# Kernel tuning notes

Measured on AMD Instinct MI355X. Metric: run time of the kernel, lower is better.

The kernel has to match this reference:

```python
import jax, jax.numpy as jnp
import numpy as np

ALPHA = 0.2   # LeakyReLU negative slope
NEG = -9e15   # mask fill value from the torch code


def _conv1d(x, w, b):
    # x: (N, C_in, L), w: (C_out, C_in, 5), padding=2 -> same length
    y = jax.lax.conv_general_dilated(x, w, window_strides=(1,), padding=[(2, 2)],
                                     dimension_numbers=('NCH', 'OIH', 'NCH'))
    return y + b[None, :, None]


def _gat(h, mask, W, a):
    # Faithful to a_input @ a: e_ij = leakyrelu(Wh_i . a[:H] + Wh_j . a[H:])
    Wh = jnp.einsum('bnf,fo->bno', h, W)          # (B,N,H)
    H = W.shape[1]
    f1 = Wh @ a[:H]                               # (B,N,1)
    f2 = Wh @ a[H:]                               # (B,N,1)
    e = f1 + jnp.swapaxes(f2, 1, 2)               # (B,N,N)
    e = jnp.where(e > 0, e, ALPHA * e)            # LeakyReLU
    e = jnp.where(mask, e, NEG)
    att = jax.nn.softmax(e, axis=-1)              # dropout skipped (eval mode)
    return jnp.einsum('bij,bjo->bio', att, Wh)


def setup_inputs() -> dict:
    key = jax.random.key(0)
    ks = jax.random.split(key, 14)
    B, S, N, H, E = 8, 200, 512, 64, 2048
    sc = 0.1
    return {
        'x': jax.random.normal(ks[0], (B, S, N * 2), dtype=jnp.float32),
        'adj': jax.random.randint(ks[1], (N, N), 0, 2, dtype=jnp.int32),
        'edge_index': jax.random.randint(ks[2], (E, 2), 0, N, dtype=jnp.int32),
        'conv1_w': jax.random.normal(ks[3], (H // 2, 2, 5), dtype=jnp.float32) * sc,
        'conv1_b': jnp.zeros((H // 2,), dtype=jnp.float32),
        'conv2_w': jax.random.normal(ks[4], (H, H // 2, 5), dtype=jnp.float32) * sc,
        'conv2_b': jnp.zeros((H,), dtype=jnp.float32),
        'W1': jax.random.normal(ks[5], (H, H), dtype=jnp.float32) * sc,
        'a1': jax.random.normal(ks[6], (2 * H, 1), dtype=jnp.float32) * sc,
        'W2': jax.random.normal(ks[7], (H, H), dtype=jnp.float32) * sc,
        'a2': jax.random.normal(ks[8], (2 * H, 1), dtype=jnp.float32) * sc,
        'fc1_w': jax.random.normal(ks[9], (2 * H, H), dtype=jnp.float32) * sc,
        'fc1_b': jnp.zeros((H,), dtype=jnp.float32),
        'fc2_w': jax.random.normal(ks[10], (H, 1), dtype=jnp.float32) * sc,
        'fc2_b': jnp.zeros((1,), dtype=jnp.float32),
    }


def reference(x, adj, edge_index, conv1_w, conv1_b, conv2_w, conv2_b,
              W1, a1, W2, a2, fc1_w, fc1_b, fc2_w, fc2_b):
    B = x.shape[0]
    N = adj.shape[0]
    # (B,S,2N) -> (B,N,S,2) -> (B*N,2,S)
    xn = x.reshape(B, -1, N, 2).transpose(0, 2, 1, 3)
    xf = xn.reshape(B * N, -1, 2).transpose(0, 2, 1)
    h = jax.nn.relu(_conv1d(xf, conv1_w, conv1_b))
    h = jax.nn.relu(_conv1d(h, conv2_w, conv2_b))
    h = h.mean(axis=-1)                 # AdaptiveAvgPool1d(1) + squeeze
    h = h.reshape(B, N, -1)             # (B,N,H)
    mask = (adj > 0)[None]              # (1,N,N) broadcasts over batch
    h = jax.nn.relu(_gat(h, mask, W1, a1))
    h = _gat(h, mask, W2, a2)
    h1 = h[:, edge_index[:, 0]]         # (B,E,H)
    h2 = h[:, edge_index[:, 1]]
    he = jnp.concatenate([h1, h2], axis=-1)  # (B,E,2H)
    z = jax.nn.relu(he @ fc1_w + fc1_b)
    return jax.nn.sigmoid(z @ fc2_w + fc2_b).squeeze(-1)  # (B,E)
```

## Files before the change

### kernel.cpp

```cpp
#include <hip/hip_runtime.h>

typedef unsigned short u16;
typedef __attribute__((ext_vector_type(8))) short short8;
typedef __attribute__((ext_vector_type(4))) float float4v;

#define BATCH 8
#define SLEN  200
#define NNODE 512
#define C1    32
#define C2    64
#define NEDGE 2048
#define NEGV  -9000000000000000.0f

#define H1S 40
#define H1R 212

__device__ __forceinline__ u16 f2bf(float f) {
    unsigned int x = __float_as_uint(f);
    unsigned int lsb = (x >> 16) & 1u;
    x += 0x7fffu + lsb;
    return (u16)(x >> 16);
}

__global__ __launch_bounds__(256) void conv_fused_kernel(
    const float* __restrict__ x,
    const float* __restrict__ w1,
    const float* __restrict__ b1,
    const float* __restrict__ w2,
    const float* __restrict__ b2,
    float* __restrict__ hmean)
{
    __shared__ float xs[2][SLEN + 4];
    __shared__ __align__(16) u16 h1p[H1R * H1S];

    const int t    = threadIdx.x;
    const int blk  = blockIdx.x;
    const int b    = blk >> 9;
    const int n    = blk & 511;
    const int lane = t & 63;
    const int wv   = t >> 6;
    const int ml   = lane & 15;
    const int q    = lane >> 4;

    short8 bfrag[5];
    {
        const float* wp = w2 + (size_t)(wv * 16 + ml) * 160 + (q * 8) * 5;
        #pragma unroll
        for (int kk = 0; kk < 5; ++kk) {
            #pragma unroll
            for (int j = 0; j < 8; ++j)
                bfrag[kk][j] = (short)f2bf(wp[j * 5 + kk]);
        }
    }
    const float bias2 = b2[wv * 16 + ml];

    if (t < SLEN) {
        const float* xp = x + ((size_t)(b * SLEN + t)) * (NNODE * 2) + n * 2;
        xs[0][2 + t] = xp[0];
        xs[1][2 + t] = xp[1];
    } else if (t < SLEN + 8) {
        int c = (t - SLEN) & 1;
        int p = (t - SLEN) >> 1;
        int pos = (p < 2) ? p : (SLEN + p);
        xs[c][pos] = 0.f;
    }
    {
        unsigned int* hz = (unsigned int*)h1p;
        if (t < 40)       hz[t] = 0u;
        else if (t < 240) hz[202 * (H1S / 2) + (t - 40)] = 0u;
    }
    __syncthreads();

    {
        const int p  = t >> 4;
        const int sg = t & 15;
        float wA[10], wB[10];
        #pragma unroll
        for (int j = 0; j < 10; ++j) {
            wA[j] = w1[(2 * p) * 10 + j];
            wB[j] = w1[(2 * p + 1) * 10 + j];
        }
        const float bA = b1[2 * p], bB = b1[2 * p + 1];
        for (int i = 0; i < 13; ++i) {
            const int s = sg + 16 * i;
            if (s < SLEN) {
                float a0 = bA, a1 = bB;
                #pragma unroll
                for (int k = 0; k < 5; ++k) {
                    const float x0 = xs[0][s + k], x1 = xs[1][s + k];
                    a0 += wA[k] * x0 + wA[5 + k] * x1;
                    a1 += wB[k] * x0 + wB[5 + k] * x1;
                }
                a0 = fmaxf(a0, 0.f);
                a1 = fmaxf(a1, 0.f);
                unsigned int pack = (unsigned int)f2bf(a0) | ((unsigned int)f2bf(a1) << 16);
                *(unsigned int*)&h1p[(2 + s) * H1S + 2 * p] = pack;
            }
        }
    }
    __syncthreads();

    float total = 0.f;
    for (int mt = 0; mt < 13; ++mt) {
        const int m0 = mt * 16;
        float4v acc = {0.f, 0.f, 0.f, 0.f};
        #pragma unroll
        for (int kk = 0; kk < 5; ++kk) {
            const short8 a = *(const short8*)&h1p[(m0 + ml + kk) * H1S + q * 8];
            acc = __builtin_amdgcn_mfma_f32_16x16x32_bf16(a, bfrag[kk], acc, 0, 0, 0);
        }
        #pragma unroll
        for (int r = 0; r < 4; ++r) {
            const int m = m0 + q * 4 + r;
            if (m < SLEN) total += fmaxf(acc[r] + bias2, 0.f);
        }
    }
    total += __shfl_xor(total, 16, 64);
    total += __shfl_xor(total, 32, 64);
    if (lane < 16)
        hmean[(size_t)blk * 64 + wv * 16 + lane] = total * (1.0f / 200.0f);
}

__global__ __launch_bounds__(256) void gat_wh_kernel(
    const float* __restrict__ h,
    const float* __restrict__ W,
    const float* __restrict__ a,
    u16* __restrict__ Wh_bt,
    float* __restrict__ f1,
    float* __restrict__ f2)
{
    __shared__ __align__(16) u16 hA[64 * 72];
    __shared__ __align__(16) u16 Wt[64 * 72];
    __shared__ __align__(16) u16 whT[64 * 72];
    __shared__ float as[128];

    const int t    = threadIdx.x;
    const int blk  = blockIdx.x;
    const int b    = blk >> 3;
    const int j0   = (blk & 7) * 64;
    const int lane = t & 63, wv = t >> 6, ml = lane & 15, q = lane >> 4;

    {
        const int r = t >> 2, c0 = (t & 3) * 16;
        const float* hp = h + ((size_t)(b * 512 + j0 + r)) * 64 + c0;
        #pragma unroll
        for (int v = 0; v < 4; ++v) {
            float4 f = *(const float4*)(hp + v * 4);
            u16* dst = &hA[r * 72 + c0 + v * 4];
            dst[0] = f2bf(f.x); dst[1] = f2bf(f.y);
            dst[2] = f2bf(f.z); dst[3] = f2bf(f.w);
        }
    }
    {
        const int k = t >> 2, o0 = (t & 3) * 16;
        const float* wp = W + k * 64 + o0;
        #pragma unroll
        for (int v = 0; v < 16; ++v)
            Wt[(o0 + v) * 72 + k] = f2bf(wp[v]);
    }
    if (t < 128) as[t] = a[t];
    __syncthreads();

    short8 af0 = *(const short8*)&hA[(16 * wv + ml) * 72 + q * 8];
    short8 af1 = *(const short8*)&hA[(16 * wv + ml) * 72 + 32 + q * 8];
    float4v acc[4];
    #pragma unroll
    for (int nt = 0; nt < 4; ++nt) {
        short8 b0 = *(const short8*)&Wt[(16 * nt + ml) * 72 + q * 8];
        short8 b1 = *(const short8*)&Wt[(16 * nt + ml) * 72 + 32 + q * 8];
        float4v c = {0.f, 0.f, 0.f, 0.f};
        c = __builtin_amdgcn_mfma_f32_16x16x32_bf16(af0, b0, c, 0, 0, 0);
        c = __builtin_amdgcn_mfma_f32_16x16x32_bf16(af1, b1, c, 0, 0, 0);
        acc[nt] = c;
    }

    #pragma unroll
    for (int nt = 0; nt < 4; ++nt)
        #pragma unroll
        for (int r = 0; r < 4; ++r)
            whT[(16 * nt + ml) * 72 + 16 * wv + q * 4 + r] = f2bf(acc[nt][r]);

    #pragma unroll
    for (int r = 0; r < 4; ++r) {
        float v1 = 0.f, v2 = 0.f;
        #pragma unroll
        for (int nt = 0; nt < 4; ++nt) {
            const float w = acc[nt][r];
            v1 += w * as[16 * nt + ml];
            v2 += w * as[64 + 16 * nt + ml];
        }
        v1 += __shfl_xor(v1, 1, 64); v2 += __shfl_xor(v2, 1, 64);
        v1 += __shfl_xor(v1, 2, 64); v2 += __shfl_xor(v2, 2, 64);
        v1 += __shfl_xor(v1, 4, 64); v2 += __shfl_xor(v2, 4, 64);
        v1 += __shfl_xor(v1, 8, 64); v2 += __shfl_xor(v2, 8, 64);
        if (ml == 0) {
            const int j = j0 + 16 * wv + q * 4 + r;
            f1[b * 512 + j] = v1;
            f2[b * 512 + j] = v2;
        }
    }
    __syncthreads();

    {
        const int o = t >> 2, js = (t & 3) * 16;
        u16* dst = Wh_bt + ((size_t)(b * 64 + o)) * 512 + j0 + js;
        *(short8*)dst = *(const short8*)&whT[o * 72 + js];
    }
}

#define PSTR 520
__global__ __launch_bounds__(256) void gat_attn_kernel(
    const u16* __restrict__ Wh_bt,
    const float* __restrict__ f1,
    const float* __restrict__ f2,
    const int* __restrict__ adj,
    float* __restrict__ outp,
    const int do_relu)
{
    __shared__ __align__(16) u16 P[16 * PSTR];
    __shared__ float f2s[512];
    __shared__ float invs[16];
    __shared__ float f1s[16];

    const int t   = threadIdx.x;
    const int blk = blockIdx.x;
    const int b   = blk >> 5;
    const int i0  = (blk & 31) * 16;

    f2s[t]       = f2[b * 512 + t];
    f2s[256 + t] = f2[b * 512 + 256 + t];
    if (t < 16) f1s[t] = f1[b * 512 + i0 + t];
    __syncthreads();

    {
        const int i = t >> 4, jseg = t & 15;
        const float f1i = f1s[i];
        const int* arow = adj + (size_t)(i0 + i) * 512 + jseg * 32;
        const float* f2p = f2s + jseg * 32;
        float ev[32];
        float mx = -3.0e38f;
        #pragma unroll
        for (int v = 0; v < 8; ++v) {
            const int4 a4 = *(const int4*)(arow + v * 4);
            #pragma unroll
            for (int u = 0; u < 4; ++u) {
                const int m = (&a4.x)[u];
                float e = f1i + f2p[v * 4 + u];
                e = e > 0.f ? e : 0.2f * e;
                e = (m > 0) ? e : NEGV;
                ev[v * 4 + u] = e;
                mx = fmaxf(mx, e);
            }
        }
        mx = fmaxf(mx, __shfl_xor(mx, 1, 64));
        mx = fmaxf(mx, __shfl_xor(mx, 2, 64));
        mx = fmaxf(mx, __shfl_xor(mx, 4, 64));
        mx = fmaxf(mx, __shfl_xor(mx, 8, 64));
        float sum = 0.f;
        #pragma unroll
        for (int v = 0; v < 32; ++v) {
            const float ex = __expf(ev[v] - mx);
            ev[v] = ex;
            sum += ex;
        }
        sum += __shfl_xor(sum, 1, 64);
        sum += __shfl_xor(sum, 2, 64);
        sum += __shfl_xor(sum, 4, 64);
        sum += __shfl_xor(sum, 8, 64);
        if (jseg == 0) invs[i] = 1.0f / sum;
        u16* prow = &P[i * PSTR + jseg * 32];
        #pragma unroll
        for (int v = 0; v < 16; ++v) {
            const unsigned int pk = (unsigned int)f2bf(ev[2 * v])
                                  | ((unsigned int)f2bf(ev[2 * v + 1]) << 16);
            *(unsigned int*)&prow[2 * v] = pk;
        }
    }
    __syncthreads();

    const int lane = t & 63, wv = t >> 6, ml = lane & 15, q = lane >> 4;
    const u16* Bp = Wh_bt + ((size_t)(b * 64 + 16 * wv + ml)) * 512 + q * 8;
    float4v acc = {0.f, 0.f, 0.f, 0.f};
    for (int ks = 0; ks < 16; ++ks) {
        const short8 afr = *(const short8*)&P[ml * PSTR + ks * 32 + q * 8];
        const short8 bfr = *(const short8*)(Bp + ks * 32);
        acc = __builtin_amdgcn_mfma_f32_16x16x32_bf16(afr, bfr, acc, 0, 0, 0);
    }
    #pragma unroll
    for (int r = 0; r < 4; ++r) {
        const int i2 = q * 4 + r;
        float val = acc[r] * invs[i2];
        if (do_relu) val = fmaxf(val, 0.f);
        outp[((size_t)(b * 512 + i0 + i2)) * 64 + 16 * wv + ml] = val;
    }
}

#define FSTR 136
__global__ __launch_bounds__(256) void edge_mlp_kernel(
    const float* __restrict__ hg,
    const int* __restrict__ eidx,
    const float* __restrict__ fc1w,
    const float* __restrict__ fc1b,
    const float* __restrict__ fc2w,
    const float* __restrict__ fc2b,
    float* __restrict__ out)
{
    __shared__ __align__(16) u16 fwT[64 * FSTR];
    __shared__ __align__(16) u16 he[16 * FSTR];
    __shared__ float part[16][4];
    __shared__ float b1s[64], w2s[64];

    const int t   = threadIdx.x;
    const int blk = blockIdx.x;
    const int b   = blk >> 7;
    const int e0  = (blk & 127) * 16;

    {
        const int k = t >> 1, o0 = (t & 1) * 32;
        const float* wp = fc1w + k * 64 + o0;
        #pragma unroll
        for (int v = 0; v < 32; ++v)
            fwT[(o0 + v) * FSTR + k] = f2bf(wp[v]);
    }
    if (t < 64) { b1s[t] = fc1b[t]; w2s[t] = fc2w[t]; }
    {
        const int ep = t >> 4, p = t & 15;
        const int e = e0 + ep;
        const int node = (p < 8) ? eidx[e * 2] : eidx[e * 2 + 1];
        const int c0 = (p & 7) * 8;
        const float* hp = hg + ((size_t)(b * 512 + node)) * 64 + c0;
        const float4 fa = *(const float4*)hp;
        const float4 fb = *(const float4*)(hp + 4);
        u16* dst = &he[ep * FSTR + ((p < 8) ? 0 : 64) + c0];
        dst[0] = f2bf(fa.x); dst[1] = f2bf(fa.y); dst[2] = f2bf(fa.z); dst[3] = f2bf(fa.w);
        dst[4] = f2bf(fb.x); dst[5] = f2bf(fb.y); dst[6] = f2bf(fb.z); dst[7] = f2bf(fb.w);
    }
    __syncthreads();

    const int lane = t & 63, wv = t >> 6, ml = lane & 15, q = lane >> 4;
    float4v acc = {0.f, 0.f, 0.f, 0.f};
    #pragma unroll
    for (int ks = 0; ks < 4; ++ks) {
        const short8 afr = *(const short8*)&he[ml * FSTR + ks * 32 + q * 8];
        const short8 bfr = *(const short8*)&fwT[(16 * wv + ml) * FSTR + ks * 32 + q * 8];
        acc = __builtin_amdgcn_mfma_f32_16x16x32_bf16(afr, bfr, acc, 0, 0, 0);
    }
    const int o = 16 * wv + ml;
    const float bo = b1s[o], wo = w2s[o];
    #pragma unroll
    for (int r = 0; r < 4; ++r) {
        float z = fmaxf(acc[r] + bo, 0.f) * wo;
        z += __shfl_xor(z, 1, 64);
        z += __shfl_xor(z, 2, 64);
        z += __shfl_xor(z, 4, 64);
        z += __shfl_xor(z, 8, 64);
        if (ml == 0) part[q * 4 + r][wv] = z;
    }
    __syncthreads();
    if (t < 16) {
        const float v = part[t][0] + part[t][1] + part[t][2] + part[t][3] + fc2b[0];
        out[b * 2048 + e0 + t] = 1.0f / (1.0f + __expf(-v));
    }
}

extern "C" void kernel_launch(void* const* d_in, const int* in_sizes, int n_in,
                              void* d_out, int out_size, void* d_ws, size_t ws_size,
                              hipStream_t stream) {
    const float* x    = (const float*)d_in[0];
    const int* adj    = (const int*)d_in[1];
    const int* eidx   = (const int*)d_in[2];
    const float* w1   = (const float*)d_in[3];
    const float* b1   = (const float*)d_in[4];
    const float* w2   = (const float*)d_in[5];
    const float* b2   = (const float*)d_in[6];
    const float* W1   = (const float*)d_in[7];
    const float* a1   = (const float*)d_in[8];
    const float* W2   = (const float*)d_in[9];
    const float* a2   = (const float*)d_in[10];
    const float* fc1w = (const float*)d_in[11];
    const float* fc1b = (const float*)d_in[12];
    const float* fc2w = (const float*)d_in[13];
    const float* fc2b = (const float*)d_in[14];
    float* out = (float*)d_out;

    float* ws = (float*)d_ws;
    const size_t R = (size_t)BATCH * NNODE;
    float* hmean = ws;
    float* g1    = hmean + R * 64;
    float* f1    = g1 + R * 64;
    float* f2    = f1 + R;
    u16*   whbt  = (u16*)(f2 + R);
    float* g2    = hmean;

    conv_fused_kernel<<<dim3(R), dim3(256), 0, stream>>>(x, w1, b1, w2, b2, hmean);
    gat_wh_kernel<<<dim3(64), dim3(256), 0, stream>>>(hmean, W1, a1, whbt, f1, f2);
    gat_attn_kernel<<<dim3(256), dim3(256), 0, stream>>>(whbt, f1, f2, adj, g1, 1);
    gat_wh_kernel<<<dim3(64), dim3(256), 0, stream>>>(g1, W2, a2, whbt, f1, f2);
    gat_attn_kernel<<<dim3(256), dim3(256), 0, stream>>>(whbt, f1, f2, adj, g2, 0);
    edge_mlp_kernel<<<dim3(1024), dim3(256), 0, stream>>>(
        g2, eidx, fc1w, fc1b, fc2w, fc2b, out);
}
```

Before: 147.1 us.

## Fuse GAT1 projection into conv kernel, run conv1 on MFMA, split attention K

A prep kernel pre-packs the conv1 and conv2 weights into bf16 MFMA fragment layout. Conv1 now runs as an im2col MFMA with split-bf16 (hi/lo) inputs and weights to keep accuracy close to fp32. The first GAT Wh projection and the f1/f2 scores are fused into the tail of the conv kernel, removing one launch and a round trip of hmean through memory. The attention kernel moves to 512 threads, splits K across wave pairs and reduces them through shared memory, and bf16 packing now uses paired conversion intrinsics. The trade-off is more per-block work and shared memory in the conv kernel, including a scalar 64x64 matvec per node.

```diff
diff --git a/kernel.cpp b/kernel.cpp
--- a/kernel.cpp
+++ b/kernel.cpp
@@ -1,4 +1,5 @@
 #include <hip/hip_runtime.h>
+#include <hip/hip_bf16.h>
 
 typedef unsigned short u16;
 typedef __attribute__((ext_vector_type(8))) short short8;
@@ -14,6 +15,7 @@
 
 #define H1S 40
 #define H1R 212
+#define A1S 32
 
 __device__ __forceinline__ u16 f2bf(float f) {
     unsigned int x = __float_as_uint(f);
@@ -22,16 +24,70 @@
     return (u16)(x >> 16);
 }
 
+__device__ __forceinline__ float bf2f(u16 u) {
+    return __uint_as_float(((unsigned int)u) << 16);
+}
+
+__device__ __forceinline__ unsigned int pk2(float a, float b) {
+    __hip_bfloat162 h = __float22bfloat162_rn(make_float2(a, b));
+    unsigned int r;
+    __builtin_memcpy(&r, &h, 4);
+    return r;
+}
+
+__global__ __launch_bounds__(256) void prep_kernel(
+    const float* __restrict__ w1,
+    const float* __restrict__ w2,
+    u16* __restrict__ w1f,
+    u16* __restrict__ w2f)
+{
+    const int t = threadIdx.x;
+    if (t < 128) {
+        const int nt = t >> 6;
+        const int l  = t & 63;
+        const int mml = l & 15, qq = l >> 4;
+        const int oc = nt * 16 + mml;
+        #pragma unroll
+        for (int j = 0; j < 8; ++j) {
+            const int k = qq * 8 + j;
+            u16 val = 0;
+            if (k < 10) {
+                val = f2bf(w1[oc * 10 + k]);
+            } else if (k < 20) {
+                val = f2bf(w1[oc * 10 + (k - 10)]);
+            } else if (k < 30) {
+                const float wf = w1[oc * 10 + (k - 20)];
+                val = f2bf(wf - bf2f(f2bf(wf)));
+            }
+            w1f[(nt * 64 + l) * 8 + j] = val;
+        }
+    }
+    const int lane = t & 63, wv = t >> 6;
+    const int ml = lane & 15, q = lane >> 4;
+    #pragma unroll
+    for (int kk = 0; kk < 5; ++kk)
+        #pragma unroll
+        for (int j = 0; j < 8; ++j)
+            w2f[((kk * 4 + wv) * 64 + lane) * 8 + j] =
+                f2bf(w2[(size_t)(wv * 16 + ml) * 160 + (q * 8 + j) * 5 + kk]);
+}
+
 __global__ __launch_bounds__(256) void conv_fused_kernel(
     const float* __restrict__ x,
-    const float* __restrict__ w1,
     const float* __restrict__ b1,
-    const float* __restrict__ w2,
     const float* __restrict__ b2,
-    float* __restrict__ hmean)
+    const float* __restrict__ W1,
+    const float* __restrict__ a1,
+    const u16* __restrict__ w1f,
+    const u16* __restrict__ w2f,
+    u16* __restrict__ Wh_bt,
+    float* __restrict__ f1,
+    float* __restrict__ f2)
 {
-    __shared__ float xs[2][SLEN + 4];
+    __shared__ __align__(16) u16 A1[208 * A1S];
     __shared__ __align__(16) u16 h1p[H1R * H1S];
+    __shared__ float hm[64];
+    __shared__ float part[4][64];
 
     const int t    = threadIdx.x;
     const int blk  = blockIdx.x;
@@ -42,83 +98,104 @@
     const int ml   = lane & 15;
     const int q    = lane >> 4;
 
-    short8 bfrag[5];
-    {
-        const float* wp = w2 + (size_t)(wv * 16 + ml) * 160 + (q * 8) * 5;
-        #pragma unroll
-        for (int kk = 0; kk < 5; ++kk) {
-            #pragma unroll
-            for (int j = 0; j < 8; ++j)
-                bfrag[kk][j] = (short)f2bf(wp[j * 5 + kk]);
-        }
-    }
-    const float bias2 = b2[wv * 16 + ml];
-
-    if (t < SLEN) {
-        const float* xp = x + ((size_t)(b * SLEN + t)) * (NNODE * 2) + n * 2;
-        xs[0][2 + t] = xp[0];
-        xs[1][2 + t] = xp[1];
-    } else if (t < SLEN + 8) {
-        int c = (t - SLEN) & 1;
-        int p = (t - SLEN) >> 1;
-        int pos = (p < 2) ? p : (SLEN + p);
-        xs[c][pos] = 0.f;
-    }
-    {
+    const short8 w1frag0 = *(const short8*)(w1f + lane * 8);
+    const short8 w1frag1 = *(const short8*)(w1f + (64 + lane) * 8);
+    short8 w2frag[5];
+    #pragma unroll
+    for (int kk = 0; kk < 5; ++kk)
+        w2frag[kk] = *(const short8*)(w2f + ((kk * 4 + wv) * 64 + lane) * 8);
+    const float bias1a = b1[ml];
+    const float bias1b = b1[16 + ml];
+    const float bias2  = b2[wv * 16 + ml];
+
+    {
+        const short8 z8 = {0, 0, 0, 0, 0, 0, 0, 0};
+        for (int idx = t; idx < 832; idx += 256) ((short8*)A1)[idx] = z8;
         unsigned int* hz = (unsigned int*)h1p;
         if (t < 40)       hz[t] = 0u;
-        else if (t < 240) hz[202 * (H1S / 2) + (t - 40)] = 0u;
-    }
-    __syncthreads();
-
-    {
-        const int p  = t >> 4;
-        const int sg = t & 15;
-        float wA[10], wB[10];
-        #pragma unroll
-        for (int j = 0; j < 10; ++j) {
-            wA[j] = w1[(2 * p) * 10 + j];
-            wB[j] = w1[(2 * p + 1) * 10 + j];
-        }
-        const float bA = b1[2 * p], bB = b1[2 * p + 1];
-        for (int i = 0; i < 13; ++i) {
-            const int s = sg + 16 * i;
-            if (s < SLEN) {
-                float a0 = bA, a1 = bB;
-                #pragma unroll
-                for (int k = 0; k < 5; ++k) {
-                    const float x0 = xs[0][s + k], x1 = xs[1][s + k];
-                    a0 += wA[k] * x0 + wA[5 + k] * x1;
-                    a1 += wB[k] * x0 + wB[5 + k] * x1;
-                }
-                a0 = fmaxf(a0, 0.f);
-                a1 = fmaxf(a1, 0.f);
-                unsigned int pack = (unsigned int)f2bf(a0) | ((unsigned int)f2bf(a1) << 16);
-                *(unsigned int*)&h1p[(2 + s) * H1S + 2 * p] = pack;
+        else if (t < 240) hz[4040 + (t - 40)] = 0u;
+    }
+    __syncthreads();
+
+    if (t < SLEN) {
+        const float2 xv = *(const float2*)(x + ((size_t)(b * SLEN + t)) * (NNODE * 2) + n * 2);
+        const u16 hx = f2bf(xv.x);
+        const u16 hy = f2bf(xv.y);
+        const u16 lx = f2bf(xv.x - bf2f(hx));
+        const u16 ly = f2bf(xv.y - bf2f(hy));
+        #pragma unroll
+        for (int kk = 0; kk < 5; ++kk) {
+            const int m = t + 2 - kk;
+            if (m >= 0) {
+                u16* row = &A1[m * A1S];
+                row[kk]      = hx;  row[5 + kk]  = hy;
+                row[10 + kk] = lx;  row[15 + kk] = ly;
+                row[20 + kk] = hx;  row[25 + kk] = hy;
             }
         }
     }
     __syncthreads();
 
+    for (int mt = wv; mt < 13; mt += 4) {
+        const short8 a = *(const short8*)&A1[(mt * 16 + ml) * A1S + q * 8];
+        float4v c0 = {0.f, 0.f, 0.f, 0.f};
+        float4v c1 = {0.f, 0.f, 0.f, 0.f};
+        c0 = __builtin_amdgcn_mfma_f32_16x16x32_bf16(a, w1frag0, c0, 0, 0, 0);
+        c1 = __builtin_amdgcn_mfma_f32_16x16x32_bf16(a, w1frag1, c1, 0, 0, 0);
+        #pragma unroll
+        for (int r = 0; r < 4; ++r) {
+            const int m = mt * 16 + q * 4 + r;
+            if (m < SLEN) {
+                h1p[(2 + m) * H1S + ml]      = f2bf(fmaxf(c0[r] + bias1a, 0.f));
+                h1p[(2 + m) * H1S + 16 + ml] = f2bf(fmaxf(c1[r] + bias1b, 0.f));
+            }
+        }
+    }
+    __syncthreads();
+
     float total = 0.f;
+    #pragma unroll
     for (int mt = 0; mt < 13; ++mt) {
-        const int m0 = mt * 16;
         float4v acc = {0.f, 0.f, 0.f, 0.f};
         #pragma unroll
         for (int kk = 0; kk < 5; ++kk) {
-            const short8 a = *(const short8*)&h1p[(m0 + ml + kk) * H1S + q * 8];
-            acc = __builtin_amdgcn_mfma_f32_16x16x32_bf16(a, bfrag[kk], acc, 0, 0, 0);
-        }
-        #pragma unroll
-        for (int r = 0; r < 4; ++r) {
-            const int m = m0 + q * 4 + r;
-            if (m < SLEN) total += fmaxf(acc[r] + bias2, 0.f);
+            const short8 a = *(const short8*)&h1p[(mt * 16 + ml + kk) * H1S + q * 8];
+            acc = __builtin_amdgcn_mfma_f32_16x16x32_bf16(a, w2frag[kk], acc, 0, 0, 0);
+        }
+        if (mt < 12) {
+            #pragma unroll
+            for (int r = 0; r < 4; ++r) total += fmaxf(acc[r] + bias2, 0.f);
+        } else if (q < 2) {
+            #pragma unroll
+            for (int r = 0; r < 4; ++r) total += fmaxf(acc[r] + bias2, 0.f);
         }
     }
     total += __shfl_xor(total, 16, 64);
     total += __shfl_xor(total, 32, 64);
-    if (lane < 16)
-        hmean[(size_t)blk * 64 + wv * 16 + lane] = total * (1.0f / 200.0f);
+    if (lane < 16) hm[wv * 16 + lane] = total * (1.0f / 200.0f);
+    __syncthreads();
+
+    {
+        const int o = t & 63, q4 = t >> 6;
+        const float* Wp = W1 + (q4 * 16) * 64 + o;
+        float p = 0.f;
+        #pragma unroll
+        for (int k = 0; k < 16; ++k) p += hm[q4 * 16 + k] * Wp[k * 64];
+        part[q4][o] = p;
+    }
+    __syncthreads();
+    if (t < 64) {
+        const float v = part[0][t] + part[1][t] + part[2][t] + part[3][t];
+        Wh_bt[((size_t)(b * 64 + t)) * 512 + n] = f2bf(v);
+        float v1 = v * a1[t];
+        float v2 = v * a1[64 + t];
+        #pragma unroll
+        for (int off = 32; off; off >>= 1) {
+            v1 += __shfl_xor(v1, off, 64);
+            v2 += __shfl_xor(v2, off, 64);
+        }
+        if (t == 0) { f1[b * 512 + n] = v1; f2[b * 512 + n] = v2; }
+    }
 }
 
 __global__ __launch_bounds__(256) void gat_wh_kernel(
@@ -146,9 +223,9 @@
         #pragma unroll
         for (int v = 0; v < 4; ++v) {
             float4 f = *(const float4*)(hp + v * 4);
-            u16* dst = &hA[r * 72 + c0 + v * 4];
-            dst[0] = f2bf(f.x); dst[1] = f2bf(f.y);
-            dst[2] = f2bf(f.z); dst[3] = f2bf(f.w);
+            unsigned int* dst = (unsigned int*)&hA[r * 72 + c0 + v * 4];
+            dst[0] = pk2(f.x, f.y);
+            dst[1] = pk2(f.z, f.w);
         }
     }
     {
@@ -175,10 +252,11 @@
     }
 
     #pragma unroll
-    for (int nt = 0; nt < 4; ++nt)
-        #pragma unroll
-        for (int r = 0; r < 4; ++r)
-            whT[(16 * nt + ml) * 72 + 16 * wv + q * 4 + r] = f2bf(acc[nt][r]);
+    for (int nt = 0; nt < 4; ++nt) {
+        unsigned int* dst = (unsigned int*)&whT[(16 * nt + ml) * 72 + 16 * wv + q * 4];
+        dst[0] = pk2(acc[nt][0], acc[nt][1]);
+        dst[1] = pk2(acc[nt][2], acc[nt][3]);
+    }
 
     #pragma unroll
     for (int r = 0; r < 4; ++r) {
@@ -209,7 +287,7 @@
 }
 
 #define PSTR 520
-__global__ __launch_bounds__(256) void gat_attn_kernel(
+__global__ __launch_bounds__(512) void gat_attn_kernel(
     const u16* __restrict__ Wh_bt,
     const float* __restrict__ f1,
     const float* __restrict__ f2,
@@ -221,33 +299,33 @@
     __shared__ float f2s[512];
     __shared__ float invs[16];
     __shared__ float f1s[16];
+    __shared__ float accH[4][64][4];
 
     const int t   = threadIdx.x;
     const int blk = blockIdx.x;
     const int b   = blk >> 5;
     const int i0  = (blk & 31) * 16;
 
-    f2s[t]       = f2[b * 512 + t];
-    f2s[256 + t] = f2[b * 512 + 256 + t];
+    f2s[t & 511] = f2[b * 512 + (t & 511)];
     if (t < 16) f1s[t] = f1[b * 512 + i0 + t];
     __syncthreads();
 
     {
-        const int i = t >> 4, jseg = t & 15;
+        const int i = t >> 5, jseg = t & 31;
         const float f1i = f1s[i];
-        const int* arow = adj + (size_t)(i0 + i) * 512 + jseg * 32;
-        const float* f2p = f2s + jseg * 32;
-        float ev[32];
+        const int* arow = adj + (size_t)(i0 + i) * 512 + jseg * 16;
+        const float* f2p = f2s + jseg * 16;
+        float ev[16];
         float mx = -3.0e38f;
         #pragma unroll
-        for (int v = 0; v < 8; ++v) {
+        for (int v = 0; v < 4; ++v) {
             const int4 a4 = *(const int4*)(arow + v * 4);
             #pragma unroll
             for (int u = 0; u < 4; ++u) {
-                const int m = (&a4.x)[u];
+                const int msk = (&a4.x)[u];
                 float e = f1i + f2p[v * 4 + u];
                 e = e > 0.f ? e : 0.2f * e;
-                e = (m > 0) ? e : NEGV;
+                e = (msk > 0) ? e : NEGV;
                 ev[v * 4 + u] = e;
                 mx = fmaxf(mx, e);
             }
@@ -256,9 +334,10 @@
         mx = fmaxf(mx, __shfl_xor(mx, 2, 64));
         mx = fmaxf(mx, __shfl_xor(mx, 4, 64));
         mx = fmaxf(mx, __shfl_xor(mx, 8, 64));
+        mx = fmaxf(mx, __shfl_xor(mx, 16, 64));
         float sum = 0.f;
         #pragma unroll
-        for (int v = 0; v < 32; ++v) {
+        for (int v = 0; v < 16; ++v) {
             const float ex = __expf(ev[v] - mx);
             ev[v] = ex;
             sum += ex;
@@ -267,31 +346,38 @@
         sum += __shfl_xor(sum, 2, 64);
         sum += __shfl_xor(sum, 4, 64);
         sum += __shfl_xor(sum, 8, 64);
+        sum += __shfl_xor(sum, 16, 64);
         if (jseg == 0) invs[i] = 1.0f / sum;
-        u16* prow = &P[i * PSTR + jseg * 32];
-        #pragma unroll
-        for (int v = 0; v < 16; ++v) {
-            const unsigned int pk = (unsigned int)f2bf(ev[2 * v])
-                                  | ((unsigned int)f2bf(ev[2 * v + 1]) << 16);
-            *(unsigned int*)&prow[2 * v] = pk;
-        }
-    }
-    __syncthreads();
-
-    const int lane = t & 63, wv = t >> 6, ml = lane & 15, q = lane >> 4;
-    const u16* Bp = Wh_bt + ((size_t)(b * 64 + 16 * wv + ml)) * 512 + q * 8;
+        unsigned int* prow = (unsigned int*)&P[i * PSTR + jseg * 16];
+        #pragma unroll
+        for (int v = 0; v < 8; ++v)
+            prow[v] = pk2(ev[2 * v], ev[2 * v + 1]);
+    }
+    __syncthreads();
+
+    const int lane = t & 63, wv = t >> 6, nt = wv & 3, kh = wv >> 2;
+    const int ml = lane & 15, q = lane >> 4;
+    const u16* Bp = Wh_bt + ((size_t)(b * 64 + nt * 16 + ml)) * 512 + kh * 256 + q * 8;
     float4v acc = {0.f, 0.f, 0.f, 0.f};
-    for (int ks = 0; ks < 16; ++ks) {
-        const short8 afr = *(const short8*)&P[ml * PSTR + ks * 32 + q * 8];
+    #pragma unroll
+    for (int ks = 0; ks < 8; ++ks) {
+        const short8 afr = *(const short8*)&P[ml * PSTR + kh * 256 + ks * 32 + q * 8];
         const short8 bfr = *(const short8*)(Bp + ks * 32);
         acc = __builtin_amdgcn_mfma_f32_16x16x32_bf16(afr, bfr, acc, 0, 0, 0);
     }
-    #pragma unroll
-    for (int r = 0; r < 4; ++r) {
-        const int i2 = q * 4 + r;
-        float val = acc[r] * invs[i2];
-        if (do_relu) val = fmaxf(val, 0.f);
-        outp[((size_t)(b * 512 + i0 + i2)) * 64 + 16 * wv + ml] = val;
+    if (kh == 1) {
+        #pragma unroll
+        for (int r = 0; r < 4; ++r) accH[nt][lane][r] = acc[r];
+    }
+    __syncthreads();
+    if (kh == 0) {
+        #pragma unroll
+        for (int r = 0; r < 4; ++r) {
+            const int i2 = q * 4 + r;
+            float val = (acc[r] + accH[nt][lane][r]) * invs[i2];
+            if (do_relu) val = fmaxf(val, 0.f);
+            outp[((size_t)(b * 512 + i0 + i2)) * 64 + nt * 16 + ml] = val;
+        }
     }
 }
 
@@ -331,9 +417,11 @@
         const float* hp = hg + ((size_t)(b * 512 + node)) * 64 + c0;
         const float4 fa = *(const float4*)hp;
         const float4 fb = *(const float4*)(hp + 4);
-        u16* dst = &he[ep * FSTR + ((p < 8) ? 0 : 64) + c0];
-        dst[0] = f2bf(fa.x); dst[1] = f2bf(fa.y); dst[2] = f2bf(fa.z); dst[3] = f2bf(fa.w);
-        dst[4] = f2bf(fb.x); dst[5] = f2bf(fb.y); dst[6] = f2bf(fb.z); dst[7] = f2bf(fb.w);
+        unsigned int* dst = (unsigned int*)&he[ep * FSTR + ((p < 8) ? 0 : 64) + c0];
+        dst[0] = pk2(fa.x, fa.y);
+        dst[1] = pk2(fa.z, fa.w);
+        dst[2] = pk2(fb.x, fb.y);
+        dst[3] = pk2(fb.z, fb.w);
     }
     __syncthreads();
 
@@ -385,18 +473,19 @@
 
     float* ws = (float*)d_ws;
     const size_t R = (size_t)BATCH * NNODE;
-    float* hmean = ws;
-    float* g1    = hmean + R * 64;
-    float* f1    = g1 + R * 64;
-    float* f2    = f1 + R;
-    u16*   whbt  = (u16*)(f2 + R);
-    float* g2    = hmean;
-
-    conv_fused_kernel<<<dim3(R), dim3(256), 0, stream>>>(x, w1, b1, w2, b2, hmean);
-    gat_wh_kernel<<<dim3(64), dim3(256), 0, stream>>>(hmean, W1, a1, whbt, f1, f2);
-    gat_attn_kernel<<<dim3(256), dim3(256), 0, stream>>>(whbt, f1, f2, adj, g1, 1);
-    gat_wh_kernel<<<dim3(64), dim3(256), 0, stream>>>(g1, W2, a2, whbt, f1, f2);
-    gat_attn_kernel<<<dim3(256), dim3(256), 0, stream>>>(whbt, f1, f2, adj, g2, 0);
+    float* g    = ws;
+    float* f1   = g + R * 64;
+    float* f2   = f1 + R;
+    u16*   whbt = (u16*)(f2 + R);
+    u16*   w1f  = whbt + R * 64;
+    u16*   w2f  = w1f + 1024;
+
+    prep_kernel<<<dim3(1), dim3(256), 0, stream>>>(w1, w2, w1f, w2f);
+    conv_fused_kernel<<<dim3(R), dim3(256), 0, stream>>>(
+        x, b1, b2, W1, a1, w1f, w2f, whbt, f1, f2);
+    gat_attn_kernel<<<dim3(256), dim3(512), 0, stream>>>(whbt, f1, f2, adj, g, 1);
+    gat_wh_kernel<<<dim3(64), dim3(256), 0, stream>>>(g, W2, a2, whbt, f1, f2);
+    gat_attn_kernel<<<dim3(256), dim3(512), 0, stream>>>(whbt, f1, f2, adj, g, 0);
     edge_mlp_kernel<<<dim3(1024), dim3(256), 0, stream>>>(
-        g2, eidx, fc1w, fc1b, fc2w, fc2b, out);
-}
+        g, eidx, fc1w, fc1b, fc2w, fc2b, out);
+}
```

New measurement: 156.8 us. 6.6% more time.
